# Performance work log

Measured on AMD Instinct MI355X. Metric: run time of the kernel, lower is better.

The kernel has to match this reference:

```python
import jax, jax.numpy as jnp
import numpy as np

N_NODES = 100000
N_EDGES = 625000
HIDDEN = 128
N_LAYERS = 4
NUM_GRAPHS = 512
INPUT_DIM = 28
EDGE_DIM = 4
OUT_DIM = 1


def setup_inputs() -> dict:
    key = jax.random.key(0)
    ks = jax.random.split(key, 16)
    x = jax.random.randint(ks[0], (N_NODES, 1), 0, INPUT_DIM)
    edge_index = jax.random.randint(ks[1], (2, N_EDGES), 0, N_NODES)
    edge_attr = jax.random.randint(ks[2], (N_EDGES,), 0, EDGE_DIM)
    batch = jnp.sort(jax.random.randint(ks[3], (N_NODES,), 0, NUM_GRAPHS))
    s = 1.0 / np.sqrt(HIDDEN)
    node_emb = jax.random.normal(ks[4], (INPUT_DIM, HIDDEN), jnp.float32)
    edge_emb = jax.random.normal(ks[5], (EDGE_DIM, HIDDEN), jnp.float32)
    conv_W1 = jax.random.normal(ks[6], (N_LAYERS, HIDDEN, HIDDEN), jnp.float32) * s
    conv_b1 = jnp.zeros((N_LAYERS, HIDDEN), jnp.float32)
    conv_W2 = jax.random.normal(ks[7], (N_LAYERS, HIDDEN, HIDDEN), jnp.float32) * s
    conv_b2 = jnp.zeros((N_LAYERS, HIDDEN), jnp.float32)
    mlp_W1 = jax.random.normal(ks[8], (HIDDEN, HIDDEN // 2), jnp.float32) * s
    mlp_b1 = jnp.zeros((HIDDEN // 2,), jnp.float32)
    mlp_W2 = jax.random.normal(ks[9], (HIDDEN // 2, HIDDEN // 4), jnp.float32) * (1.0 / np.sqrt(HIDDEN // 2))
    mlp_b2 = jnp.zeros((HIDDEN // 4,), jnp.float32)
    mlp_W3 = jax.random.normal(ks[10], (HIDDEN // 4, OUT_DIM), jnp.float32) * (1.0 / np.sqrt(HIDDEN // 4))
    mlp_b3 = jnp.zeros((OUT_DIM,), jnp.float32)
    return dict(x=x, edge_index=edge_index, edge_attr=edge_attr, batch=batch,
                node_emb=node_emb, edge_emb=edge_emb,
                conv_W1=conv_W1, conv_b1=conv_b1, conv_W2=conv_W2, conv_b2=conv_b2,
                mlp_W1=mlp_W1, mlp_b1=mlp_b1, mlp_W2=mlp_W2, mlp_b2=mlp_b2,
                mlp_W3=mlp_W3, mlp_b3=mlp_b3)


def reference(x, edge_index, edge_attr, batch, node_emb, edge_emb,
              conv_W1, conv_b1, conv_W2, conv_b2,
              mlp_W1, mlp_b1, mlp_W2, mlp_b2, mlp_W3, mlp_b3):
    h = node_emb[x[:, 0]]                    # [N, H] embedding lookup (x.squeeze(-1))
    _attr = edge_emb[edge_attr]              # computed in original forward but unused by GINConv
    src, dst = edge_index[0], edge_index[1]
    for l in range(N_LAYERS):
        # GINConv (eps=0): mlp((1+eps)*x + sum_{j->i} x_j)
        agg = jax.ops.segment_sum(h[src], dst, num_segments=N_NODES)  # [N, H]
        z = agg + h
        z = jax.nn.relu(z @ conv_W1[l] + conv_b1[l])
        h = z @ conv_W2[l] + conv_b2[l]
    g = jax.ops.segment_sum(h, batch, num_segments=NUM_GRAPHS)        # global_add_pool [G, H]
    g = jax.nn.relu(g @ mlp_W1 + mlp_b1)
    g = jax.nn.relu(g @ mlp_W2 + mlp_b2)
    return g @ mlp_W3 + mlp_b3               # [G, 1]
```

## Files before the change

kernel.cpp:

```cpp
#include <hip/hip_runtime.h>

#define N_NODES 100000
#define N_EDGES 625000
#define HIDDEN 128
#define NUM_GRAPHS 512
#define CAP 40
#define PADN 100096

typedef unsigned int uint;
typedef unsigned short ushort;
typedef short v8s __attribute__((ext_vector_type(8)));
typedef float v16f __attribute__((ext_vector_type(16)));

__device__ __forceinline__ float b2f_lo(uint u) { return __uint_as_float(u << 16); }
__device__ __forceinline__ float b2f_hi(uint u) { return __uint_as_float(u & 0xffff0000u); }
__device__ __forceinline__ uint f2b(float f) {
  uint u = __float_as_uint(f);
  return (u + 0x7fffu + ((u >> 16) & 1u)) >> 16;
}

__global__ __launch_bounds__(256) void wtrans_k(const float* __restrict__ W1,
                                                const float* __restrict__ W2,
                                                ushort* __restrict__ Wt) {
  int mat = blockIdx.x;
  const float* W = ((mat & 1) ? W2 : W1) + (size_t)(mat >> 1) * 16384;
  ushort* o = Wt + (size_t)mat * 16384;
#pragma unroll
  for (int j = 0; j < 64; j++) {
    int idx = threadIdx.x + 256 * j;
    int k = idx >> 7, n = idx & 127;
    int c = n >> 5, l31 = n & 31;
    int ks = k >> 4, khalf = (k >> 3) & 1, e = k & 7;
    o[(((c * 8 + ks) << 6) + (khalf << 5) + l31) * 8 + e] = (ushort)f2b(W[idx]);
  }
}

__global__ __launch_bounds__(256) void embed_k(const int* __restrict__ x,
                                               const float* __restrict__ emb,
                                               ushort* __restrict__ h) {
  int t = blockIdx.x * 256 + threadIdx.x;
  int n = t >> 4;
  if (n >= N_NODES) return;
  int c = t & 15;
  const float4* e = (const float4*)(emb + (size_t)x[n] * HIDDEN + c * 8);
  float4 a = e[0], b = e[1];
  uint4 o;
  o.x = f2b(a.x) | (f2b(a.y) << 16);
  o.y = f2b(a.z) | (f2b(a.w) << 16);
  o.z = f2b(b.x) | (f2b(b.y) << 16);
  o.w = f2b(b.z) | (f2b(b.w) << 16);
  ((uint4*)h)[t] = o;
}

__global__ __launch_bounds__(256) void build_k(const int* __restrict__ src,
                                               const int* __restrict__ dst,
                                               int* __restrict__ cursor,
                                               int* __restrict__ slots) {
  int e = blockIdx.x * 256 + threadIdx.x;
  if (e >= N_EDGES) return;
  int d = dst[e];
  int p = atomicAdd(&cursor[d], 1);
  if (p < CAP) slots[(size_t)d * CAP + p] = src[e];
}

__global__ __launch_bounds__(256) void hist_k(const int* __restrict__ cursor,
                                              int* __restrict__ bins) {
  __shared__ int lb[CAP + 1];
  int tid = threadIdx.x;
  if (tid <= CAP) lb[tid] = 0;
  __syncthreads();
  int n = blockIdx.x * 256 + tid;
  if (n < N_NODES) {
    int d = cursor[n]; if (d > CAP) d = CAP;
    atomicAdd(&lb[d], 1);
  }
  __syncthreads();
  if (tid <= CAP && lb[tid] > 0) atomicAdd(&bins[tid], lb[tid]);
}

__global__ __launch_bounds__(64) void scan_k(int* __restrict__ bins) {
  int i = threadIdx.x;
  int c = (i <= CAP) ? bins[i] : 0;
  int incl = c;
#pragma unroll
  for (int off = 1; off < 64; off <<= 1) {
    int t = __shfl_up(incl, off, 64);
    if (i >= off) incl += t;
  }
  if (i <= CAP) bins[i] = incl - c;
}

__global__ __launch_bounds__(256) void scatter_k(const int* __restrict__ cursor,
                                                 int* __restrict__ bins,
                                                 int* __restrict__ perm) {
  __shared__ int lb[CAP + 1];
  __shared__ int lbase[CAP + 1];
  int tid = threadIdx.x;
  if (tid <= CAP) lb[tid] = 0;
  __syncthreads();
  int n = blockIdx.x * 256 + tid;
  int d = 0, rank = 0;
  bool real = (n < N_NODES);
  if (real) {
    d = cursor[n]; if (d > CAP) d = CAP;
    rank = atomicAdd(&lb[d], 1);
  }
  __syncthreads();
  if (tid <= CAP) {
    int c = lb[tid];
    lbase[tid] = c > 0 ? atomicAdd(&bins[tid], c) : 0;
  }
  __syncthreads();
  if (real) perm[lbase[d] + rank] = n;
  else if (n < PADN) perm[n] = 0;
}

__device__ __forceinline__ void accum8(const uint4 u[8], float acc[8][8]) {
#pragma unroll
  for (int ks = 0; ks < 8; ks++) {
    acc[ks][0] += b2f_lo(u[ks].x); acc[ks][1] += b2f_hi(u[ks].x);
    acc[ks][2] += b2f_lo(u[ks].y); acc[ks][3] += b2f_hi(u[ks].y);
    acc[ks][4] += b2f_lo(u[ks].z); acc[ks][5] += b2f_hi(u[ks].z);
    acc[ks][6] += b2f_lo(u[ks].w); acc[ks][7] += b2f_hi(u[ks].w);
  }
}

__global__ __launch_bounds__(64, 3) void layer_k(const ushort* __restrict__ hin,
                                                 const int* __restrict__ cursor,
                                                 const int* __restrict__ slots,
                                                 const int* __restrict__ perm,
                                                 const ushort* __restrict__ W1f,
                                                 const ushort* __restrict__ W2f,
                                                 const float* __restrict__ b1,
                                                 const float* __restrict__ b2,
                                                 ushort* __restrict__ hout) {
  int lane = threadIdx.x;
  int l31 = lane & 31;
  int khalf = lane >> 5;
  int tb = blockIdx.x * 32;
  int prow = perm[tb + l31];
  bool valid = (tb + l31) < N_NODES;

  float acc[8][8];
#pragma unroll
  for (int ks = 0; ks < 8; ks++)
#pragma unroll
    for (int e = 0; e < 8; e++) acc[ks][e] = 0.f;

  const uint4* base = (const uint4*)hin;
  uint4 cur[8], nxt[8];
  const uint4* rp = base + (size_t)prow * 16;
#pragma unroll
  for (int ks = 0; ks < 8; ks++) cur[ks] = rp[khalf + 2 * ks];

  int deg = valid ? cursor[prow] : 0;
  if (deg > CAP) deg = CAP;
  const int* sl = slots + (size_t)prow * CAP;
  int s = (deg > 0) ? sl[0] : 0;
  for (int j = 0; j < deg; j++) {
    const uint4* np = base + (size_t)s * 16;
#pragma unroll
    for (int ks = 0; ks < 8; ks++) nxt[ks] = np[khalf + 2 * ks];
    s = (j + 1 < deg) ? sl[j + 1] : 0;
    accum8(cur, acc);
#pragma unroll
    for (int ks = 0; ks < 8; ks++) cur[ks] = nxt[ks];
  }
  accum8(cur, acc);

  union U { uint4 u; v8s s; };
  U afr[8];
#pragma unroll
  for (int ks = 0; ks < 8; ks++) {
    afr[ks].u.x = f2b(acc[ks][0]) | (f2b(acc[ks][1]) << 16);
    afr[ks].u.y = f2b(acc[ks][2]) | (f2b(acc[ks][3]) << 16);
    afr[ks].u.z = f2b(acc[ks][4]) | (f2b(acc[ks][5]) << 16);
    afr[ks].u.w = f2b(acc[ks][6]) | (f2b(acc[ks][7]) << 16);
  }

  const uint4* W1v = (const uint4*)W1f;
  v16f acc1[4] = {};
#pragma unroll
  for (int c = 0; c < 4; c++)
#pragma unroll
    for (int ks = 0; ks < 8; ks++) {
      U b; b.u = W1v[((c * 8 + ks) << 6) + lane];
      acc1[c] = __builtin_amdgcn_mfma_f32_32x32x16_bf16(b.s, afr[ks].s, acc1[c], 0, 0, 0);
    }

  uint u[4][4][2];
#pragma unroll
  for (int c = 0; c < 4; c++)
#pragma unroll
    for (int b = 0; b < 4; b++)
#pragma unroll
      for (int ap = 0; ap < 2; ap++) {
        int r0 = 2 * ap + 4 * b, r1 = r0 + 1;
        float v0 = fmaxf(acc1[c][r0] + b1[c * 32 + 2 * ap + 8 * b + 4 * khalf], 0.f);
        float v1 = fmaxf(acc1[c][r1] + b1[c * 32 + 2 * ap + 1 + 8 * b + 4 * khalf], 0.f);
        u[c][b][ap] = f2b(v0) | (f2b(v1) << 16);
      }

  uint got[4][2][2];
#pragma unroll
  for (int c = 0; c < 4; c++)
#pragma unroll
    for (int bh = 0; bh < 2; bh++)
#pragma unroll
      for (int ap = 0; ap < 2; ap++) {
        uint send = khalf ? u[c][2 * bh][ap] : u[c][2 * bh + 1][ap];
        got[c][bh][ap] = __shfl_xor(send, 32, 64);
      }

  U az[8];
#pragma unroll
  for (int ks = 0; ks < 8; ks++) {
    uint o0 = khalf ? u[ks >> 1][2 * (ks & 1) + 1][0] : u[ks >> 1][2 * (ks & 1)][0];
    uint o1 = khalf ? u[ks >> 1][2 * (ks & 1) + 1][1] : u[ks >> 1][2 * (ks & 1)][1];
    uint g0 = got[ks >> 1][ks & 1][0];
    uint g1 = got[ks >> 1][ks & 1][1];
    az[ks].u.x = khalf ? g0 : o0;
    az[ks].u.y = khalf ? g1 : o1;
    az[ks].u.z = khalf ? o0 : g0;
    az[ks].u.w = khalf ? o1 : g1;
  }

  const uint4* W2v = (const uint4*)W2f;
  v16f acc2[4] = {};
#pragma unroll
  for (int c = 0; c < 4; c++)
#pragma unroll
    for (int ks = 0; ks < 8; ks++) {
      U b; b.u = W2v[((c * 8 + ks) << 6) + lane];
      acc2[c] = __builtin_amdgcn_mfma_f32_32x32x16_bf16(az[ks].s, b.s, acc2[c], 0, 0, 0);
    }

  int trow[16];
#pragma unroll
  for (int r = 0; r < 16; r++) {
    int m = (r & 3) + 8 * (r >> 2) + 4 * khalf;
    trow[r] = __shfl(prow, m, 64);
  }
  float bv2[4];
#pragma unroll
  for (int c = 0; c < 4; c++) bv2[c] = b2[c * 32 + l31];
#pragma unroll
  for (int c = 0; c < 4; c++) {
    int col = c * 32 + l31;
#pragma unroll
    for (int r = 0; r < 16; r++) {
      int m = (r & 3) + 8 * (r >> 2) + 4 * khalf;
      if (tb + m < N_NODES)
        hout[(size_t)trow[r] * HIDDEN + col] = (ushort)f2b(acc2[c][r] + bv2[c]);
    }
  }
}

__global__ __launch_bounds__(256) void poolmlp_k(const ushort* __restrict__ h,
                                                 const int* __restrict__ batch,
                                                 const float* __restrict__ W1, const float* __restrict__ b1,
                                                 const float* __restrict__ W2, const float* __restrict__ b2,
                                                 const float* __restrict__ W3, const float* __restrict__ b3,
                                                 float* __restrict__ out) {
  __shared__ int se[2];
  __shared__ float red[16][16][8];
  __shared__ float gl[128];
  __shared__ float r2[64];
  __shared__ float r3[32];
  int gi = blockIdx.x, tid = threadIdx.x;
  if (tid < 2) {
    int target = gi + tid;
    int lo = 0, hi = N_NODES;
    while (lo < hi) {
      int mid = (lo + hi) >> 1;
      if (batch[mid] < target) lo = mid + 1; else hi = mid;
    }
    se[tid] = lo;
  }
  __syncthreads();
  int start = se[0], end = se[1];
  int cg = tid & 15, rg = tid >> 4;
  float acc[8] = {0.f, 0.f, 0.f, 0.f, 0.f, 0.f, 0.f, 0.f};
  for (int r = start + rg; r < end; r += 16) {
    uint4 v = ((const uint4*)h)[r * 16 + cg];
    acc[0] += b2f_lo(v.x); acc[1] += b2f_hi(v.x);
    acc[2] += b2f_lo(v.y); acc[3] += b2f_hi(v.y);
    acc[4] += b2f_lo(v.z); acc[5] += b2f_hi(v.z);
    acc[6] += b2f_lo(v.w); acc[7] += b2f_hi(v.w);
  }
#pragma unroll
  for (int j = 0; j < 8; j++) red[rg][cg][j] = acc[j];
  __syncthreads();
  if (rg == 0) {
    float s[8];
#pragma unroll
    for (int j = 0; j < 8; j++) s[j] = red[0][cg][j];
#pragma unroll
    for (int i = 1; i < 16; i++)
#pragma unroll
      for (int j = 0; j < 8; j++) s[j] += red[i][cg][j];
#pragma unroll
    for (int j = 0; j < 8; j++) gl[cg * 8 + j] = s[j];
  }
  __syncthreads();
  if (tid < 64) {
    float s = b1[tid];
    for (int k = 0; k < 128; k++) s = fmaf(gl[k], W1[k * 64 + tid], s);
    r2[tid] = fmaxf(s, 0.f);
  }
  __syncthreads();
  if (tid < 32) {
    float s2 = b2[tid];
    for (int k = 0; k < 64; k++) s2 = fmaf(r2[k], W2[k * 32 + tid], s2);
    r3[tid] = fmaxf(s2, 0.f);
  }
  __syncthreads();
  if (tid < 64) {
    float pv = (tid < 32) ? r3[tid] * W3[tid] : 0.f;
#pragma unroll
    for (int off = 32; off > 0; off >>= 1) pv += __shfl_down(pv, off);
    if (tid == 0) out[gi] = pv + b3[0];
  }
}

extern "C" void kernel_launch(void* const* d_in, const int* in_sizes, int n_in,
                              void* d_out, int out_size, void* d_ws, size_t ws_size,
                              hipStream_t stream) {
  const int* x = (const int*)d_in[0];
  const int* src = (const int*)d_in[1];
  const int* dst = src + N_EDGES;
  const int* batch = (const int*)d_in[3];
  const float* node_emb = (const float*)d_in[4];
  const float* cW1 = (const float*)d_in[6];
  const float* cb1 = (const float*)d_in[7];
  const float* cW2 = (const float*)d_in[8];
  const float* cb2 = (const float*)d_in[9];
  const float* mW1 = (const float*)d_in[10];
  const float* mb1 = (const float*)d_in[11];
  const float* mW2 = (const float*)d_in[12];
  const float* mb2 = (const float*)d_in[13];
  const float* mW3 = (const float*)d_in[14];
  const float* mb3 = (const float*)d_in[15];
  float* out = (float*)d_out;

  char* p = (char*)d_ws;
  const size_t HB = (size_t)N_NODES * HIDDEN * sizeof(ushort);
  ushort* h = (ushort*)p;      p += HB;
  ushort* t0 = (ushort*)p;     p += HB;
  ushort* Wtb = (ushort*)p;    p += (size_t)8 * 16384 * sizeof(ushort);
  int* cursor = (int*)p;       p += (size_t)N_NODES * sizeof(int);
  int* bins = (int*)p;         p += 64 * sizeof(int);
  int* slots = (int*)p;        p += (size_t)N_NODES * CAP * sizeof(int);
  int* perm = (int*)p;         p += (size_t)PADN * sizeof(int);

  hipMemsetAsync(cursor, 0, ((size_t)N_NODES + 64) * sizeof(int), stream);
  wtrans_k<<<8, 256, 0, stream>>>(cW1, cW2, Wtb);
  embed_k<<<(N_NODES * 16 + 255) / 256, 256, 0, stream>>>(x, node_emb, h);
  build_k<<<(N_EDGES + 255) / 256, 256, 0, stream>>>(src, dst, cursor, slots);
  hist_k<<<PADN / 256, 256, 0, stream>>>(cursor, bins);
  scan_k<<<1, 64, 0, stream>>>(bins);
  scatter_k<<<PADN / 256, 256, 0, stream>>>(cursor, bins, perm);

  const int grid = PADN / 32;
  ushort* bufs[2] = {h, t0};
  for (int l = 0; l < 4; l++) {
    layer_k<<<grid, 64, 0, stream>>>(bufs[l & 1], cursor, slots, perm,
                                     Wtb + (size_t)(2 * l) * 16384,
                                     Wtb + (size_t)(2 * l + 1) * 16384,
                                     cb1 + (size_t)l * HIDDEN,
                                     cb2 + (size_t)l * HIDDEN,
                                     bufs[(l & 1) ^ 1]);
  }
  poolmlp_k<<<NUM_GRAPHS, 256, 0, stream>>>(h, batch, mW1, mb1, mW2, mb2, mW3, mb3, out);
}
```

Before: 363.1 us.

## Ping-pong neighbor row buffers with sched barriers and reverse degree-sorted node order

After: 355.7 us. -2.0%, faster.

```diff
diff --git a/kernel.cpp b/kernel.cpp
--- a/kernel.cpp
+++ b/kernel.cpp
@@ -111,8 +111,14 @@
     lbase[tid] = c > 0 ? atomicAdd(&bins[tid], c) : 0;
   }
   __syncthreads();
-  if (real) perm[lbase[d] + rank] = n;
+  if (real) perm[(N_NODES - 1) - (lbase[d] + rank)] = n;
   else if (n < PADN) perm[n] = 0;
+}
+
+__device__ __forceinline__ void loadrow(uint4 dst[8], const uint4* __restrict__ rowp,
+                                        int khalf) {
+#pragma unroll
+  for (int ks = 0; ks < 8; ks++) dst[ks] = rowp[khalf + 2 * ks];
 }
 
 __device__ __forceinline__ void accum8(const uint4 u[8], float acc[8][8]) {
@@ -148,25 +154,27 @@
     for (int e = 0; e < 8; e++) acc[ks][e] = 0.f;
 
   const uint4* base = (const uint4*)hin;
-  uint4 cur[8], nxt[8];
-  const uint4* rp = base + (size_t)prow * 16;
-#pragma unroll
-  for (int ks = 0; ks < 8; ks++) cur[ks] = rp[khalf + 2 * ks];
+  uint4 A[8], B[8];
+  loadrow(A, base + (size_t)prow * 16, khalf);
 
   int deg = valid ? cursor[prow] : 0;
   if (deg > CAP) deg = CAP;
   const int* sl = slots + (size_t)prow * CAP;
-  int s = (deg > 0) ? sl[0] : 0;
-  for (int j = 0; j < deg; j++) {
-    const uint4* np = base + (size_t)s * 16;
-#pragma unroll
-    for (int ks = 0; ks < 8; ks++) nxt[ks] = np[khalf + 2 * ks];
-    s = (j + 1 < deg) ? sl[j + 1] : 0;
-    accum8(cur, acc);
-#pragma unroll
-    for (int ks = 0; ks < 8; ks++) cur[ks] = nxt[ks];
-  }
-  accum8(cur, acc);
+  if (deg > 0) loadrow(B, base + (size_t)sl[0] * 16, khalf);
+  __builtin_amdgcn_sched_barrier(0);
+  accum8(A, acc);
+
+  int j = 0;
+  while (j + 2 <= deg) {
+    loadrow(A, base + (size_t)sl[j + 1] * 16, khalf);
+    __builtin_amdgcn_sched_barrier(0);
+    accum8(B, acc);
+    if (j + 2 < deg) loadrow(B, base + (size_t)sl[j + 2] * 16, khalf);
+    __builtin_amdgcn_sched_barrier(0);
+    accum8(A, acc);
+    j += 2;
+  }
+  if (j < deg) accum8(B, acc);
 
   union U { uint4 u; v8s s; };
   U afr[8];
```
